# Kernel optimization log

Measured on AMD Instinct MI355X. Metric: run time of the kernel, lower is better.

The kernel has to match this reference:

```python
import jax, jax.numpy as jnp
import numpy as np

B, NL2, NRC, NIN = 32768, 4, 8, 41
NCTRL = NIN + NL2 + NIN  # 86


def _blur(n):
    # tridiagonal blur: 0.8 on diag, 0.1 on the two off-diagonals (symmetric)
    return 0.8 * jnp.eye(n, dtype=jnp.float32) \
         + 0.1 * jnp.eye(n, k=1, dtype=jnp.float32) \
         + 0.1 * jnp.eye(n, k=-1, dtype=jnp.float32)


def _leaky(x):
    return jnp.where(x >= 0, x, 0.2 * x)  # LeakyReLU(0.2)


def _passgate(w, b, rc, x):
    # w: [B,out,in,rc] clamped to [-1,1]; rc: [B,rc]; x: [B,in] -> [B,out]
    w2 = jnp.einsum('boir,br->boi', jnp.clip(w, -1.0, 1.0), rc)
    return jnp.einsum('boi,bi->bo', w2, x) + b


def setup_inputs() -> dict:
    key = jax.random.key(0)
    ks = jax.random.split(key, 4)
    s_f = np.float32(np.sqrt(2.0 / (NIN * NRC)))
    s_r = np.float32(np.sqrt(2.0 / (NL2 * NRC)))
    inp = jax.random.normal(ks[0], (B, NIN), dtype=jnp.float32)
    fpg_w = jnp.clip(jax.random.normal(ks[1], (B, NL2, NIN, NRC), dtype=jnp.float32) * s_f, -1.0, 1.0)
    rpg_w = jnp.clip(jax.random.normal(ks[2], (B, NIN, NL2, NRC), dtype=jnp.float32) * s_r, -1.0, 1.0)
    fpg_b = jnp.zeros((B, NL2), dtype=jnp.float32)
    rpg_b = jnp.zeros((B, NIN), dtype=jnp.float32)
    # pgctrl: shared nn.Linear(86, 8) (default torch init ~ U(-1/sqrt(86), 1/sqrt(86)))
    bound = np.float32(1.0 / np.sqrt(NCTRL))
    kw, kb = jax.random.split(ks[3])
    pgctrl_w = jax.random.uniform(kw, (NRC, NCTRL), dtype=jnp.float32, minval=-bound, maxval=bound)
    pgctrl_b = jax.random.uniform(kb, (NRC,), dtype=jnp.float32, minval=-bound, maxval=bound)
    return {"inp": inp, "fpg_w": fpg_w, "fpg_b": fpg_b,
            "rpg_w": rpg_w, "rpg_b": rpg_b,
            "pgctrl_w": pgctrl_w, "pgctrl_b": pgctrl_b}


def reference(inp, fpg_w, fpg_b, rpg_w, rpg_b, pgctrl_w, pgctrl_b):
    rcblur = _blur(NRC)   # [8,8]
    l2blur = _blur(NL2)   # [4,4]
    # initial state buffers are zeros; note l2old/rcold are NOT updated inside
    # the outer loop (faithful to the original), only l1i carries over.
    l2old = jnp.zeros((B, NL2), dtype=inp.dtype)
    rcold = jnp.zeros((B, NRC), dtype=inp.dtype)
    l1i = jnp.zeros((B, NIN), dtype=inp.dtype)
    l2 = l2old
    rc = rcold
    for _ in range(2):
        rcin = jnp.concatenate([inp, l2old, inp - l1i], axis=1)  # [B,86]
        rc = _leaky(rcin @ pgctrl_w.T + pgctrl_b)
        rc = jnp.clip(0.4 * rc + 0.6 * rcold, -0.2, 1.0)
        for _ in range(3):
            rc = rc @ rcblur.T
        l2 = _passgate(fpg_w, fpg_b, rc, inp) * 0.1 + 0.9 * l2old
        l2 = jnp.clip(l2, -0.2, 1.0)
        for _ in range(2):
            l2 = l2 @ l2blur.T
        l1i = jnp.clip(_passgate(rpg_w, rpg_b, rc, l2), -0.2, 1.0)
    return (l1i, l2, rc)
```

## Files before the change

kernel.cpp:

```cpp
#include <hip/hip_runtime.h>

#define B_ROWS 32768
#define NIN 41
#define NL2 4
#define NRC 8

__device__ __forceinline__ float med3(float v, float lo, float hi) {
    return __builtin_amdgcn_fmed3f(v, lo, hi);
}

template <int Ctrl>
__device__ __forceinline__ int dpp_add(int x) {
    return __float_as_int(
        __int_as_float(x) +
        __int_as_float(__builtin_amdgcn_update_dpp(0, x, Ctrl, 0xf, 0xf, true)));
}

__device__ __forceinline__ float wave_sum_uniform(float v) {
    int x = __float_as_int(v);
    x = dpp_add<0x111>(x);
    x = dpp_add<0x112>(x);
    x = dpp_add<0x114>(x);
    x = dpp_add<0x118>(x);
    x = dpp_add<0x142>(x);
    x = dpp_add<0x143>(x);
    return __int_as_float(__builtin_amdgcn_readlane(x, 63));
}

__device__ __forceinline__ void blur8(float* v) {
    float t[NRC];
    #pragma unroll
    for (int r = 0; r < NRC; ++r) {
        float s = 0.8f * v[r];
        if (r > 0)       s += 0.1f * v[r - 1];
        if (r < NRC - 1) s += 0.1f * v[r + 1];
        t[r] = s;
    }
    #pragma unroll
    for (int r = 0; r < NRC; ++r) v[r] = t[r];
}

__device__ __forceinline__ void blur4(float* v) {
    float t[NL2];
    #pragma unroll
    for (int o = 0; o < NL2; ++o) {
        float s = 0.8f * v[o];
        if (o > 0)       s += 0.1f * v[o - 1];
        if (o < NL2 - 1) s += 0.1f * v[o + 1];
        t[o] = s;
    }
    #pragma unroll
    for (int o = 0; o < NL2; ++o) v[o] = t[o];
}

__global__ void __launch_bounds__(256, 8) pgnet_kernel(
    const float* __restrict__ inp,
    const float* __restrict__ fpg_w,
    const float* __restrict__ fpg_b,
    const float* __restrict__ rpg_w,
    const float* __restrict__ rpg_b,
    const float* __restrict__ pgw,
    const float* __restrict__ pgb,
    float* __restrict__ out)
{
    const int lane = threadIdx.x & 63;
    const int row  = blockIdx.x * 4 + (threadIdx.x >> 6);
    const bool act = lane < NIN;
    const int safe = act ? lane : (NIN - 1);

    const float x_raw = inp[row * NIN + safe];

    float w1r[NRC], w2r[NRC];
    #pragma unroll
    for (int r = 0; r < NRC; ++r) {
        w1r[r] = pgw[r * 86 + safe];
        w2r[r] = pgw[r * 86 + 45 + safe];
    }

    const float* fp = fpg_w + (size_t)row * 1312 + (size_t)safe * 8;
    float4 fwv[NL2][2];
    #pragma unroll
    for (int o = 0; o < NL2; ++o) {
        fwv[o][0] = *(const float4*)(fp + o * 328);
        fwv[o][1] = *(const float4*)(fp + o * 328 + 4);
    }

    const float4 fbv  = *(const float4*)(fpg_b + (size_t)row * NL2);
    const float  rb_r = rpg_b[row * NIN + safe];

    __builtin_amdgcn_sched_barrier(0);

    const float x  = act ? x_raw : 0.0f;
    const float rb = act ? rb_r  : 0.0f;

    float W2[NRC], A[NRC];
    #pragma unroll
    for (int r = 0; r < NRC; ++r) {
        A[r]  = wave_sum_uniform(x * (w1r[r] + w2r[r])) + pgb[r];
        W2[r] = act ? w2r[r] : 0.0f;
    }

    float F[NL2][NRC];
    #pragma unroll
    for (int o = 0; o < NL2; ++o) {
        const float f0 = x * med3(fwv[o][0].x, -1.f, 1.f);
        const float f1 = x * med3(fwv[o][0].y, -1.f, 1.f);
        const float f2 = x * med3(fwv[o][0].z, -1.f, 1.f);
        const float f3 = x * med3(fwv[o][0].w, -1.f, 1.f);
        const float f4 = x * med3(fwv[o][1].x, -1.f, 1.f);
        const float f5 = x * med3(fwv[o][1].y, -1.f, 1.f);
        const float f6 = x * med3(fwv[o][1].z, -1.f, 1.f);
        const float f7 = x * med3(fwv[o][1].w, -1.f, 1.f);
        F[o][0] = wave_sum_uniform(f0); F[o][1] = wave_sum_uniform(f1);
        F[o][2] = wave_sum_uniform(f2); F[o][3] = wave_sum_uniform(f3);
        F[o][4] = wave_sum_uniform(f4); F[o][5] = wave_sum_uniform(f5);
        F[o][6] = wave_sum_uniform(f6); F[o][7] = wave_sum_uniform(f7);
    }

    const float* rp = rpg_w + (size_t)row * 1312 + (size_t)safe * 32;
    float4 rwv[8];
    #pragma unroll
    for (int j = 0; j < 8; ++j) rwv[j] = ((const float4*)rp)[j];
    __builtin_amdgcn_sched_barrier(0);

    const float fb[NL2] = {fbv.x, fbv.y, fbv.z, fbv.w};

    float rcv[NRC];
    #pragma unroll
    for (int r = 0; r < NRC; ++r) {
        const float pre = A[r];
        const float v = (pre >= 0.f) ? pre : 0.2f * pre;
        rcv[r] = med3(0.4f * v, -0.2f, 1.0f);
    }
    blur8(rcv); blur8(rcv); blur8(rcv);

    float l2v[NL2];
    #pragma unroll
    for (int o = 0; o < NL2; ++o) {
        float s = fb[o];
        #pragma unroll
        for (int r = 0; r < NRC; ++r) s += F[o][r] * rcv[r];
        l2v[o] = med3(0.1f * s, -0.2f, 1.0f);
    }
    blur4(l2v); blur4(l2v);

    float rw[NL2][NRC];
    #pragma unroll
    for (int o = 0; o < NL2; ++o) {
        rw[o][0] = med3(rwv[2*o].x, -1.f, 1.f);   rw[o][1] = med3(rwv[2*o].y, -1.f, 1.f);
        rw[o][2] = med3(rwv[2*o].z, -1.f, 1.f);   rw[o][3] = med3(rwv[2*o].w, -1.f, 1.f);
        rw[o][4] = med3(rwv[2*o+1].x, -1.f, 1.f); rw[o][5] = med3(rwv[2*o+1].y, -1.f, 1.f);
        rw[o][6] = med3(rwv[2*o+1].z, -1.f, 1.f); rw[o][7] = med3(rwv[2*o+1].w, -1.f, 1.f);
    }

    float l1;
    {
        float acc = rb;
        #pragma unroll
        for (int o = 0; o < NL2; ++o) {
            float d = 0.f;
            #pragma unroll
            for (int r = 0; r < NRC; ++r) d += rw[o][r] * rcv[r];
            acc += l2v[o] * d;
        }
        l1 = med3(acc, -0.2f, 1.0f);
    }

    #pragma unroll
    for (int r = 0; r < NRC; ++r) {
        const float pre = A[r] - wave_sum_uniform(l1 * W2[r]);
        const float v = (pre >= 0.f) ? pre : 0.2f * pre;
        rcv[r] = med3(0.4f * v, -0.2f, 1.0f);
    }
    blur8(rcv); blur8(rcv); blur8(rcv);

    #pragma unroll
    for (int o = 0; o < NL2; ++o) {
        float s = fb[o];
        #pragma unroll
        for (int r = 0; r < NRC; ++r) s += F[o][r] * rcv[r];
        l2v[o] = med3(0.1f * s, -0.2f, 1.0f);
    }
    blur4(l2v); blur4(l2v);

    {
        float acc = rb;
        #pragma unroll
        for (int o = 0; o < NL2; ++o) {
            float d = 0.f;
            #pragma unroll
            for (int r = 0; r < NRC; ++r) d += rw[o][r] * rcv[r];
            acc += l2v[o] * d;
        }
        l1 = med3(acc, -0.2f, 1.0f);
    }

    if (act) out[(size_t)row * NIN + lane] = l1;
    if (lane < NL2) {
        float v = l2v[0];
        #pragma unroll
        for (int o = 1; o < NL2; ++o) if (lane == o) v = l2v[o];
        out[(size_t)B_ROWS * NIN + (size_t)row * NL2 + lane] = v;
    }
    if (lane < NRC) {
        float v = rcv[0];
        #pragma unroll
        for (int r = 1; r < NRC; ++r) if (lane == r) v = rcv[r];
        out[(size_t)B_ROWS * (NIN + NL2) + (size_t)row * NRC + lane] = v;
    }
}

extern "C" void kernel_launch(void* const* d_in, const int* in_sizes, int n_in,
                              void* d_out, int out_size, void* d_ws, size_t ws_size,
                              hipStream_t stream) {
    const float* inp   = (const float*)d_in[0];
    const float* fpg_w = (const float*)d_in[1];
    const float* fpg_b = (const float*)d_in[2];
    const float* rpg_w = (const float*)d_in[3];
    const float* rpg_b = (const float*)d_in[4];
    const float* pgw   = (const float*)d_in[5];
    const float* pgb   = (const float*)d_in[6];
    float* out = (float*)d_out;

    dim3 grid(B_ROWS / 4);
    dim3 block(256);
    hipLaunchKernelGGL(pgnet_kernel, grid, block, 0, stream,
                       inp, fpg_w, fpg_b, rpg_w, rpg_b, pgw, pgb, out);
}
```

Measured before the change: 421.8 us.

## Reduce fpg passgate after contracting with rc, cutting wave reductions

Rather than precomputing 32 cross-lane wave sums of x*clamped forward weights, each lane now contracts its clamped forward weights with rc locally and does one wave reduction per output, 4 per iteration and 8 in total. This cuts the DPP/readlane reduction work, which was the dominant ALU cost. It also issues both weight-tensor loads up front and relaxes the launch bounds from 8 to 4 waves per EU, so the compiler can use more registers. The trade-off is lower guaranteed occupancy for a memory-heavy kernel, and a different floating-point summation order.

```diff
diff --git a/kernel.cpp b/kernel.cpp
--- a/kernel.cpp
+++ b/kernel.cpp
@@ -53,7 +53,7 @@
     for (int o = 0; o < NL2; ++o) v[o] = t[o];
 }
 
-__global__ void __launch_bounds__(256, 8) pgnet_kernel(
+__global__ void __launch_bounds__(256, 4) pgnet_kernel(
     const float* __restrict__ inp,
     const float* __restrict__ fpg_w,
     const float* __restrict__ fpg_b,
@@ -70,6 +70,19 @@
 
     const float x_raw = inp[row * NIN + safe];
 
+    const float* fp = fpg_w + (size_t)row * 1312 + (size_t)safe * 8;
+    float4 fwv[NL2][2];
+    #pragma unroll
+    for (int o = 0; o < NL2; ++o) {
+        fwv[o][0] = *(const float4*)(fp + o * 328);
+        fwv[o][1] = *(const float4*)(fp + o * 328 + 4);
+    }
+
+    const float* rp = rpg_w + (size_t)row * 1312 + (size_t)safe * 32;
+    float4 rwv[8];
+    #pragma unroll
+    for (int j = 0; j < 8; ++j) rwv[j] = ((const float4*)rp)[j];
+
     float w1r[NRC], w2r[NRC];
     #pragma unroll
     for (int r = 0; r < NRC; ++r) {
@@ -77,14 +90,6 @@
         w2r[r] = pgw[r * 86 + 45 + safe];
     }
 
-    const float* fp = fpg_w + (size_t)row * 1312 + (size_t)safe * 8;
-    float4 fwv[NL2][2];
-    #pragma unroll
-    for (int o = 0; o < NL2; ++o) {
-        fwv[o][0] = *(const float4*)(fp + o * 328);
-        fwv[o][1] = *(const float4*)(fp + o * 328 + 4);
-    }
-
     const float4 fbv  = *(const float4*)(fpg_b + (size_t)row * NL2);
     const float  rb_r = rpg_b[row * NIN + safe];
 
@@ -100,50 +105,14 @@
         W2[r] = act ? w2r[r] : 0.0f;
     }
 
-    float F[NL2][NRC];
-    #pragma unroll
-    for (int o = 0; o < NL2; ++o) {
-        const float f0 = x * med3(fwv[o][0].x, -1.f, 1.f);
-        const float f1 = x * med3(fwv[o][0].y, -1.f, 1.f);
-        const float f2 = x * med3(fwv[o][0].z, -1.f, 1.f);
-        const float f3 = x * med3(fwv[o][0].w, -1.f, 1.f);
-        const float f4 = x * med3(fwv[o][1].x, -1.f, 1.f);
-        const float f5 = x * med3(fwv[o][1].y, -1.f, 1.f);
-        const float f6 = x * med3(fwv[o][1].z, -1.f, 1.f);
-        const float f7 = x * med3(fwv[o][1].w, -1.f, 1.f);
-        F[o][0] = wave_sum_uniform(f0); F[o][1] = wave_sum_uniform(f1);
-        F[o][2] = wave_sum_uniform(f2); F[o][3] = wave_sum_uniform(f3);
-        F[o][4] = wave_sum_uniform(f4); F[o][5] = wave_sum_uniform(f5);
-        F[o][6] = wave_sum_uniform(f6); F[o][7] = wave_sum_uniform(f7);
-    }
-
-    const float* rp = rpg_w + (size_t)row * 1312 + (size_t)safe * 32;
-    float4 rwv[8];
-    #pragma unroll
-    for (int j = 0; j < 8; ++j) rwv[j] = ((const float4*)rp)[j];
-    __builtin_amdgcn_sched_barrier(0);
-
-    const float fb[NL2] = {fbv.x, fbv.y, fbv.z, fbv.w};
-
-    float rcv[NRC];
-    #pragma unroll
-    for (int r = 0; r < NRC; ++r) {
-        const float pre = A[r];
-        const float v = (pre >= 0.f) ? pre : 0.2f * pre;
-        rcv[r] = med3(0.4f * v, -0.2f, 1.0f);
-    }
-    blur8(rcv); blur8(rcv); blur8(rcv);
-
-    float l2v[NL2];
-    #pragma unroll
-    for (int o = 0; o < NL2; ++o) {
-        float s = fb[o];
-        #pragma unroll
-        for (int r = 0; r < NRC; ++r) s += F[o][r] * rcv[r];
-        l2v[o] = med3(0.1f * s, -0.2f, 1.0f);
-    }
-    blur4(l2v); blur4(l2v);
-
+    float fw[NL2][NRC];
+    #pragma unroll
+    for (int o = 0; o < NL2; ++o) {
+        fw[o][0] = med3(fwv[o][0].x, -1.f, 1.f); fw[o][1] = med3(fwv[o][0].y, -1.f, 1.f);
+        fw[o][2] = med3(fwv[o][0].z, -1.f, 1.f); fw[o][3] = med3(fwv[o][0].w, -1.f, 1.f);
+        fw[o][4] = med3(fwv[o][1].x, -1.f, 1.f); fw[o][5] = med3(fwv[o][1].y, -1.f, 1.f);
+        fw[o][6] = med3(fwv[o][1].z, -1.f, 1.f); fw[o][7] = med3(fwv[o][1].w, -1.f, 1.f);
+    }
     float rw[NL2][NRC];
     #pragma unroll
     for (int o = 0; o < NL2; ++o) {
@@ -153,7 +122,28 @@
         rw[o][6] = med3(rwv[2*o+1].z, -1.f, 1.f); rw[o][7] = med3(rwv[2*o+1].w, -1.f, 1.f);
     }
 
-    float l1;
+    const float fb[NL2] = {fbv.x, fbv.y, fbv.z, fbv.w};
+
+    float l1, rcv[NRC], l2v[NL2];
+
+    #pragma unroll
+    for (int r = 0; r < NRC; ++r) {
+        const float pre = A[r];
+        const float v = (pre >= 0.f) ? pre : 0.2f * pre;
+        rcv[r] = med3(0.4f * v, -0.2f, 1.0f);
+    }
+    blur8(rcv); blur8(rcv); blur8(rcv);
+
+    #pragma unroll
+    for (int o = 0; o < NL2; ++o) {
+        float d = 0.f;
+        #pragma unroll
+        for (int r = 0; r < NRC; ++r) d += fw[o][r] * rcv[r];
+        const float s = wave_sum_uniform(x * d) + fb[o];
+        l2v[o] = med3(0.1f * s, -0.2f, 1.0f);
+    }
+    blur4(l2v); blur4(l2v);
+
     {
         float acc = rb;
         #pragma unroll
@@ -176,9 +166,10 @@
 
     #pragma unroll
     for (int o = 0; o < NL2; ++o) {
-        float s = fb[o];
-        #pragma unroll
-        for (int r = 0; r < NRC; ++r) s += F[o][r] * rcv[r];
+        float d = 0.f;
+        #pragma unroll
+        for (int r = 0; r < NRC; ++r) d += fw[o][r] * rcv[r];
+        const float s = wave_sum_uniform(x * d) + fb[o];
         l2v[o] = med3(0.1f * s, -0.2f, 1.0f);
     }
     blur4(l2v); blur4(l2v);
```

After: 358.0 us. 1.18x faster.
